# Optimization experiments

Measured on AMD Instinct MI355X. Metric: run time of the kernel, lower is better.

The kernel has to match this reference:

```python
import jax, jax.numpy as jnp
import numpy as np

B, T, D, H = 2, 2048, 1024, 16
HD = D // H  # 64


def setup_inputs() -> dict:
    key = jax.random.key(0)
    ks = jax.random.split(key, 9)
    w = lambda k, shp: (jax.random.normal(k, shp, jnp.float32) * 0.02)
    return {
        "x": jax.random.normal(ks[0], (B, T, D), jnp.float32),
        "Wq": w(ks[1], (D, D)), "bq": jnp.zeros((D,), jnp.float32),
        "Wk": w(ks[2], (D, D)), "bk": jnp.zeros((D,), jnp.float32),
        "Wv": w(ks[3], (D, D)), "bv": jnp.zeros((D,), jnp.float32),
        "Wo": w(ks[4], (D, D)), "bo": jnp.zeros((D,), jnp.float32),
        "Wqs": w(ks[5], (3, HD)), "bqs": jnp.zeros((3,), jnp.float32),
        "Wks": w(ks[6], (3, HD)), "bks": jnp.zeros((3,), jnp.float32),
        "Wvs": w(ks[7], (3, HD)), "bvs": jnp.zeros((3,), jnp.float32),
        "temp": jnp.float32(1.0),
    }


def reference(x, Wq, bq, Wk, bk, Wv, bv, Wo, bo, Wqs, bqs, Wks, bks, Wvs, bvs, temp):
    Bx, Tx, Dx = x.shape
    # project and split heads: [B,H,T,HD]
    split = lambda y: y.reshape(Bx, Tx, H, HD).transpose(0, 2, 1, 3)
    q = split(x @ Wq.T + bq)
    k = split(x @ Wk.T + bk)
    v = split(x @ Wv.T + bv)
    # STP projections to 3-d: [B,H,T,3]
    q_stp = q @ Wqs.T + bqs
    k3 = k @ Wks.T + bks
    v3 = v @ Wvs.T + bvs
    # cross-product term (note: original's layernormed k_sub/v_sub are dead code)
    cross_kv = jnp.cross(k3, v3, axis=-1)  # [B,H,T,3]
    scores = (jnp.einsum('bhqd,bhkd->bhqk', q, k)
              + jnp.einsum('bhqc,bhkc->bhqk', q_stp, cross_kv)) * temp
    attn = jax.nn.softmax(scores, axis=-1)
    out = jnp.einsum('bhqk,bhkd->bhqd', attn, v)  # [B,H,T,HD]
    out = out.transpose(0, 2, 1, 3).reshape(Bx, Tx, Dx)
    return out @ Wo.T + bo
```

## Files before the change

kernel.cpp:

```cpp
#include <hip/hip_runtime.h>
#include <stdint.h>

typedef unsigned short u16;
typedef unsigned int u32;
typedef __attribute__((ext_vector_type(8))) short bf16x8;
typedef __attribute__((ext_vector_type(4))) float f32x4;

__device__ __forceinline__ u16 f2b(float f) {
    union { float f; u32 u; } t; t.f = f;
    return (u16)((t.u + 0x7FFFu + ((t.u >> 16) & 1u)) >> 16);
}
__device__ __forceinline__ float b2f(u16 h) {
    union { u32 u; float f; } t; t.u = ((u32)h) << 16;
    return t.f;
}
__device__ __forceinline__ u32 pack2(float a, float b) {
    return (u32)f2b(a) | ((u32)f2b(b) << 16);
}

__device__ __forceinline__ void async_cp16(const u16* g, const u16* lds_base) {
    __builtin_amdgcn_global_load_lds(
        (const __attribute__((address_space(1))) void*)(uintptr_t)g,
        (__attribute__((address_space(3))) void*)(u32)(uintptr_t)lds_base,
        16, 0, 0);
}

__global__ void cast_all_kernel(const float* __restrict__ x,
                                const float* __restrict__ Wq, const float* __restrict__ Wk,
                                const float* __restrict__ Wv, const float* __restrict__ Wo,
                                u16* __restrict__ xb, u16* __restrict__ Wqb, u16* __restrict__ Wkb,
                                u16* __restrict__ Wvb, u16* __restrict__ Wob) {
    int i = blockIdx.x * blockDim.x + threadIdx.x;
    const float* s; u16* d; int off;
    if (i < 1048576) { s = x; d = xb; off = i; }
    else {
        int j = i - 1048576;
        int w = j >> 18; off = j & 262143;
        if (w == 0) { s = Wq; d = Wqb; }
        else if (w == 1) { s = Wk; d = Wkb; }
        else if (w == 2) { s = Wv; d = Wvb; }
        else { s = Wo; d = Wob; }
    }
    float4 f = ((const float4*)s)[off];
    ((uint2*)d)[off] = make_uint2(pack2(f.x, f.y), pack2(f.z, f.w));
}

#define GT 128
#define GK 32

template<int MODE>
__device__ __forceinline__ void gemm_core(
    const u16* __restrict__ A, const u16* __restrict__ W, const float* __restrict__ bias,
    u16* __restrict__ obf, u16* __restrict__ vtout, float* __restrict__ ofp)
{
    __shared__ __align__(16) u16 As[GT * GK];
    __shared__ __align__(16) u16 Bs[GT * GK];
    const int tid = threadIdx.x;
    const int lane = tid & 63, w = tid >> 6;
    const int wm = w >> 1, wn = w & 1;
    const int l15 = lane & 15, quad = lane >> 4;
    const int M0 = blockIdx.y * GT, N0 = blockIdx.x * GT;

    f32x4 acc[4][4];
#pragma unroll
    for (int i = 0; i < 4; i++)
#pragma unroll
        for (int j = 0; j < 4; j++) acc[i][j] = (f32x4){0.f, 0.f, 0.f, 0.f};

    int ua = w * 128 + lane;
    int r0 = ua >> 2, c0 = ((ua & 3) ^ (r0 & 3)) * 8;
    int ub = ua + 64;
    int r1 = ub >> 2, c1 = ((ub & 3) ^ (r1 & 3)) * 8;
    const u16* Ag0 = A + (size_t)(M0 + r0) * 1024 + c0;
    const u16* Ag1 = A + (size_t)(M0 + r1) * 1024 + c1;
    const u16* Wg0 = W + (size_t)(N0 + r0) * 1024 + c0;
    const u16* Wg1 = W + (size_t)(N0 + r1) * 1024 + c1;
    const u16* As0 = As + (w * 128) * 8;
    const u16* As1 = As + (w * 128 + 64) * 8;
    const u16* Bs0 = Bs + (w * 128) * 8;
    const u16* Bs1 = Bs + (w * 128 + 64) * 8;

    for (int k0 = 0; k0 < 1024; k0 += GK) {
        __syncthreads();
        async_cp16(Ag0 + k0, As0);
        async_cp16(Ag1 + k0, As1);
        async_cp16(Wg0 + k0, Bs0);
        async_cp16(Wg1 + k0, Bs1);
        __syncthreads();

        bf16x8 af[4], bf[4];
#pragma unroll
        for (int mi = 0; mi < 4; mi++)
            af[mi] = *(const bf16x8*)(As + (wm * 64 + mi * 16 + l15) * 32 + ((quad ^ (l15 & 3)) * 8));
#pragma unroll
        for (int ni = 0; ni < 4; ni++)
            bf[ni] = *(const bf16x8*)(Bs + (wn * 64 + ni * 16 + l15) * 32 + ((quad ^ (l15 & 3)) * 8));
#pragma unroll
        for (int mi = 0; mi < 4; mi++)
#pragma unroll
            for (int ni = 0; ni < 4; ni++)
                acc[mi][ni] = __builtin_amdgcn_mfma_f32_16x16x32_bf16(af[mi], bf[ni], acc[mi][ni], 0, 0, 0);
    }

#pragma unroll
    for (int mi = 0; mi < 4; mi++)
#pragma unroll
        for (int ni = 0; ni < 4; ni++) {
            int n = N0 + wn * 64 + ni * 16 + l15;
            float bias_n = bias[n];
            float vals[4];
#pragma unroll
            for (int r = 0; r < 4; r++)
                vals[r] = acc[mi][ni][r] + bias_n;
            int m0 = M0 + wm * 64 + mi * 16 + quad * 4;
            if (MODE == 0) {
                int b = m0 >> 11, t = m0 & 2047;
                int h = n >> 6, hd = n & 63;
#pragma unroll
                for (int r = 0; r < 4; r++)
                    obf[((size_t)((b * 16 + h) * 2048 + (t + r)) << 6) + hd] = f2b(vals[r]);
                if (vtout) {
                    *(uint2*)(vtout + ((size_t)((b * 16 + h) * 64 + hd)) * 2048 + t) =
                        make_uint2(pack2(vals[0], vals[1]), pack2(vals[2], vals[3]));
                }
            } else {
#pragma unroll
                for (int r = 0; r < 4; r++)
                    ofp[(size_t)(m0 + r) * 1024 + n] = vals[r];
            }
        }
}

__global__ __launch_bounds__(256) void gemm_qkv_kernel(
    const u16* __restrict__ xb,
    const u16* __restrict__ Wq, const u16* __restrict__ Wk, const u16* __restrict__ Wv,
    const float* __restrict__ bq, const float* __restrict__ bk, const float* __restrict__ bv,
    u16* __restrict__ q, u16* __restrict__ k, u16* __restrict__ v, u16* __restrict__ vT)
{
    const u16* W; const float* bias; u16* o; u16* vt = nullptr;
    if (blockIdx.z == 0)      { W = Wq; bias = bq; o = q; }
    else if (blockIdx.z == 1) { W = Wk; bias = bk; o = k; }
    else                      { W = Wv; bias = bv; o = v; vt = vT; }
    gemm_core<0>(xb, W, bias, o, vt, nullptr);
}

__global__ __launch_bounds__(256) void gemm_out_kernel(
    const u16* __restrict__ ao, const u16* __restrict__ Wo, const float* __restrict__ bo,
    float* __restrict__ out)
{
    gemm_core<1>(ao, Wo, bo, nullptr, nullptr, out);
}

__global__ void build_ext_kernel(
    const u16* __restrict__ q, const u16* __restrict__ k, const u16* __restrict__ v,
    const float* __restrict__ Wqs, const float* __restrict__ bqs,
    const float* __restrict__ Wks, const float* __restrict__ bks,
    const float* __restrict__ Wvs, const float* __restrict__ bvs,
    const float* __restrict__ temp_p,
    u16* __restrict__ qe, u16* __restrict__ ke)
{
    int row = blockIdx.x * blockDim.x + threadIdx.x;
    if (row >= 2 * 16 * 2048) return;
    const float temp = *temp_p * 1.44269504088896f;
    const u16* qr = q + (size_t)row * 64;
    const u16* kr = k + (size_t)row * 64;
    const u16* vr = v + (size_t)row * 64;

    float qs0 = bqs[0], qs1 = bqs[1], qs2 = bqs[2];
    float ks0 = bks[0], ks1 = bks[1], ks2 = bks[2];
    float vs0 = bvs[0], vs1 = bvs[1], vs2 = bvs[2];
#pragma unroll
    for (int j = 0; j < 64; j += 8) {
        bf16x8 qv = *(const bf16x8*)(qr + j);
        bf16x8 kv = *(const bf16x8*)(kr + j);
        bf16x8 vv = *(const bf16x8*)(vr + j);
#pragma unroll
        for (int i = 0; i < 8; i++) {
            float qf = b2f((u16)qv[i]);
            float kf = b2f((u16)kv[i]);
            float vf = b2f((u16)vv[i]);
            qs0 += qf * Wqs[j + i]; qs1 += qf * Wqs[64 + j + i]; qs2 += qf * Wqs[128 + j + i];
            ks0 += kf * Wks[j + i]; ks1 += kf * Wks[64 + j + i]; ks2 += kf * Wks[128 + j + i];
            vs0 += vf * Wvs[j + i]; vs1 += vf * Wvs[64 + j + i]; vs2 += vf * Wvs[128 + j + i];
        }
    }
    float c0 = ks1 * vs2 - ks2 * vs1;
    float c1 = ks2 * vs0 - ks0 * vs2;
    float c2 = ks0 * vs1 - ks1 * vs0;

    u16* qer = qe + (size_t)row * 96;
    u16* ker = ke + (size_t)row * 96;
#pragma unroll
    for (int j = 0; j < 64; j += 8) {
        bf16x8 qv = *(const bf16x8*)(qr + j);
        bf16x8 sq;
#pragma unroll
        for (int i = 0; i < 8; i++) sq[i] = (short)f2b(b2f((u16)qv[i]) * temp);
        *(bf16x8*)(qer + j) = sq;
        *(bf16x8*)(ker + j) = *(const bf16x8*)(kr + j);
    }
    *(uint2*)(qer + 64) = make_uint2(pack2(qs0 * temp, qs1 * temp), (u32)f2b(qs2 * temp));
    *(uint2*)(ker + 64) = make_uint2(pack2(c0, c1), (u32)f2b(c2));
    uint2 z = make_uint2(0u, 0u);
#pragma unroll
    for (int j = 68; j < 96; j += 4) {
        *(uint2*)(qer + j) = z;
        *(uint2*)(ker + j) = z;
    }
}

__global__ __launch_bounds__(256) void attn_kernel(
    const u16* __restrict__ qe, const u16* __restrict__ ke, const u16* __restrict__ vT,
    u16* __restrict__ out)
{
    __shared__ __align__(16) u16 Ks[64 * 128];
    __shared__ __align__(16) u16 Vt[64 * 64];
    __shared__ __align__(16) u16 Ps[128 * 64];

    const int tid = threadIdx.x;
    const int lane = tid & 63, w = tid >> 6;
    const int l15 = lane & 15, quad = lane >> 4;
    const int lsw = l15 & 7;
    const int bh = blockIdx.y;
    const int q0 = blockIdx.x * 128;

    const u16* qeb = qe + (size_t)bh * 2048 * 96;
    const u16* keb = ke + (size_t)bh * 2048 * 96;
    const u16* vTb = vT + (size_t)bh * 64 * 2048;

    bf16x8 bq[2][3];
#pragma unroll
    for (int s = 0; s < 2; s++) {
        const u16* qrow = qeb + (size_t)(q0 + w * 32 + s * 16 + l15) * 96;
#pragma unroll
        for (int ks = 0; ks < 3; ks++) bq[s][ks] = *(const bf16x8*)(qrow + ks * 32 + quad * 8);
    }

    f32x4 O[2][4];
    float l_part[2];
#pragma unroll
    for (int s = 0; s < 2; s++) {
        l_part[s] = 0.f;
#pragma unroll
        for (int dt = 0; dt < 4; dt++) O[s][dt] = (f32x4){0.f, 0.f, 0.f, 0.f};
    }

    const int srow = tid >> 2, spart = tid & 3;
    const int sh = srow & 7;
    u16* Pw[2];
#pragma unroll
    for (int s = 0; s < 2; s++) Pw[s] = Ps + (size_t)(w * 32 + s * 16 + l15) * 64;

    for (int kb = 0; kb < 2048; kb += 64) {
        const u16* kg = keb + (size_t)(kb + srow) * 96;
        uint4 kx0 = *(const uint4*)(kg + spart * 8);
        uint4 kx1 = *(const uint4*)(kg + (spart + 4) * 8);
        uint4 kx2 = *(const uint4*)(kg + (spart + 8) * 8);
        const u16* vg = vTb + (size_t)srow * 2048 + kb;
        uint4 vx0 = *(const uint4*)(vg + spart * 8);
        uint4 vx1 = *(const uint4*)(vg + (spart + 4) * 8);
        __syncthreads();
        *(uint4*)(Ks + srow * 128 + ((spart    ) ^ sh) * 8) = kx0;
        *(uint4*)(Ks + srow * 128 + ((spart + 4) ^ sh) * 8) = kx1;
        *(uint4*)(Ks + srow * 128 + ((spart + 8) ^ sh) * 8) = kx2;
        *(uint4*)(Vt + srow * 64 + ((spart    ) ^ sh) * 8) = vx0;
        *(uint4*)(Vt + srow * 64 + ((spart + 4) ^ sh) * 8) = vx1;
        __syncthreads();

        f32x4 S[2][4];
#pragma unroll
        for (int s = 0; s < 2; s++)
#pragma unroll
            for (int nt = 0; nt < 4; nt++) S[s][nt] = (f32x4){0.f, 0.f, 0.f, 0.f};
#pragma unroll
        for (int ks = 0; ks < 3; ks++) {
            bf16x8 ak[4];
#pragma unroll
            for (int nt = 0; nt < 4; nt++)
                ak[nt] = *(const bf16x8*)(Ks + (nt * 16 + l15) * 128 + (((ks * 4 + quad) ^ lsw) & 15) * 8);
#pragma unroll
            for (int s = 0; s < 2; s++)
#pragma unroll
                for (int nt = 0; nt < 4; nt++)
                    S[s][nt] = __builtin_amdgcn_mfma_f32_16x16x32_bf16(ak[nt], bq[s][ks], S[s][nt], 0, 0, 0);
        }

#pragma unroll
        for (int s = 0; s < 2; s++) {
            float sum = 0.f;
#pragma unroll
            for (int nt = 0; nt < 4; nt++)
#pragma unroll
                for (int r = 0; r < 4; r++) {
                    float p = __builtin_amdgcn_exp2f(S[s][nt][r]);
                    S[s][nt][r] = p;
                    sum += p;
                }
            l_part[s] += sum;
#pragma unroll
            for (int nt = 0; nt < 4; nt++) {
                int c = (nt * 2 + (quad >> 1)) ^ lsw;
                *(uint2*)(Pw[s] + c * 8 + (quad & 1) * 4) =
                    make_uint2(pack2(S[s][nt][0], S[s][nt][1]), pack2(S[s][nt][2], S[s][nt][3]));
            }
        }

#pragma unroll
        for (int kk = 0; kk < 2; kk++) {
            bf16x8 av[4];
#pragma unroll
            for (int dt = 0; dt < 4; dt++)
                av[dt] = *(const bf16x8*)(Vt + (dt * 16 + l15) * 64 + ((kk * 4 + quad) ^ lsw) * 8);
#pragma unroll
            for (int s = 0; s < 2; s++) {
                bf16x8 pb = *(const bf16x8*)(Pw[s] + ((kk * 4 + quad) ^ lsw) * 8);
#pragma unroll
                for (int dt = 0; dt < 4; dt++)
                    O[s][dt] = __builtin_amdgcn_mfma_f32_16x16x32_bf16(av[dt], pb, O[s][dt], 0, 0, 0);
            }
        }
    }

    const int b = bh >> 4, h = bh & 15;
#pragma unroll
    for (int s = 0; s < 2; s++) {
        float l = l_part[s];
        l += __shfl_xor(l, 16);
        l += __shfl_xor(l, 32);
        float linv = 1.0f / l;
        int tq = q0 + w * 32 + s * 16 + l15;
#pragma unroll
        for (int dt = 0; dt < 4; dt++) {
            int d = h * 64 + dt * 16 + quad * 4;
            *(uint2*)(out + (size_t)(b * 2048 + tq) * 1024 + d) =
                make_uint2(pack2(O[s][dt][0] * linv, O[s][dt][1] * linv),
                           pack2(O[s][dt][2] * linv, O[s][dt][3] * linv));
        }
    }
}

extern "C" void kernel_launch(void* const* d_in, const int* in_sizes, int n_in,
                              void* d_out, int out_size, void* d_ws, size_t ws_size,
                              hipStream_t stream)
{
    (void)in_sizes; (void)n_in; (void)out_size; (void)ws_size;
    const float* x   = (const float*)d_in[0];
    const float* Wq  = (const float*)d_in[1];
    const float* bq  = (const float*)d_in[2];
    const float* Wk  = (const float*)d_in[3];
    const float* bk  = (const float*)d_in[4];
    const float* Wv  = (const float*)d_in[5];
    const float* bv  = (const float*)d_in[6];
    const float* Wo  = (const float*)d_in[7];
    const float* bo  = (const float*)d_in[8];
    const float* Wqs = (const float*)d_in[9];
    const float* bqs = (const float*)d_in[10];
    const float* Wks = (const float*)d_in[11];
    const float* bks = (const float*)d_in[12];
    const float* Wvs = (const float*)d_in[13];
    const float* bvs = (const float*)d_in[14];
    const float* temp = (const float*)d_in[15];

    char* ws = (char*)d_ws;
    u16* xb  = (u16*)(ws);
    u16* Wqb = (u16*)(ws + 8388608);
    u16* Wkb = (u16*)(ws + 10485760);
    u16* Wvb = (u16*)(ws + 12582912);
    u16* Wob = (u16*)(ws + 14680064);
    u16* qb  = (u16*)(ws + 16777216);
    u16* kbq = (u16*)(ws + 25165824);
    u16* vbq = (u16*)(ws + 33554432);
    u16* qeb = (u16*)(ws + 41943040);
    u16* keb = (u16*)(ws + 54525952);
    u16* vTb = (u16*)(ws + 67108864);
    u16* aob = xb;

    cast_all_kernel<<<8192, 256, 0, stream>>>(x, Wq, Wk, Wv, Wo, xb, Wqb, Wkb, Wvb, Wob);
    gemm_qkv_kernel<<<dim3(8, 32, 3), 256, 0, stream>>>(xb, Wqb, Wkb, Wvb, bq, bk, bv, qb, kbq, vbq, vTb);
    build_ext_kernel<<<256, 256, 0, stream>>>(qb, kbq, vbq, Wqs, bqs, Wks, bks, Wvs, bvs, temp, qeb, keb);
    attn_kernel<<<dim3(16, 32), 256, 0, stream>>>(qeb, keb, vTb, aob);
    gemm_out_kernel<<<dim3(8, 32), 256, 0, stream>>>(aob, Wob, bo, (float*)d_out);
}
```

Baseline: 253.4 us.

## Fuse STP projections into QKV GEMM epilogue and shrink output GEMM tile

The QKV GEMM epilogue now computes the 3-d STP projections with a cross-lane shuffle reduction and writes the extended q/k rows and transposed V directly. This removes the separate q/k/v bf16 buffers and the build_ext pass that re-read them. A small finish kernel computes the k×v cross product from float4 side buffers. Separately, the output GEMM uses 64x128 tiles to launch twice as many blocks, trading less per-block reuse for better CU occupancy. The epilogue stores are scalar u16 writes with per-row zero padding, which may be less coalesced than before.

```diff
diff --git a/kernel.cpp b/kernel.cpp
--- a/kernel.cpp
+++ b/kernel.cpp
@@ -9,10 +9,6 @@
 __device__ __forceinline__ u16 f2b(float f) {
     union { float f; u32 u; } t; t.f = f;
     return (u16)((t.u + 0x7FFFu + ((t.u >> 16) & 1u)) >> 16);
-}
-__device__ __forceinline__ float b2f(u16 h) {
-    union { u32 u; float f; } t; t.u = ((u32)h) << 16;
-    return t.f;
 }
 __device__ __forceinline__ u32 pack2(float a, float b) {
     return (u32)f2b(a) | ((u32)f2b(b) << 16);
@@ -45,21 +41,30 @@
     ((uint2*)d)[off] = make_uint2(pack2(f.x, f.y), pack2(f.z, f.w));
 }
 
-#define GT 128
-#define GK 32
-
-template<int MODE>
-__device__ __forceinline__ void gemm_core(
-    const u16* __restrict__ A, const u16* __restrict__ W, const float* __restrict__ bias,
-    u16* __restrict__ obf, u16* __restrict__ vtout, float* __restrict__ ofp)
+__global__ __launch_bounds__(256) void gemm_qkv_kernel(
+    const u16* __restrict__ xb,
+    const u16* __restrict__ Wq, const u16* __restrict__ Wk, const u16* __restrict__ Wv,
+    const float* __restrict__ bq, const float* __restrict__ bk, const float* __restrict__ bv,
+    const float* __restrict__ Wqs, const float* __restrict__ bqs,
+    const float* __restrict__ Wks, const float* __restrict__ bks,
+    const float* __restrict__ Wvs, const float* __restrict__ bvs,
+    const float* __restrict__ temp_p,
+    u16* __restrict__ qe, u16* __restrict__ ke, u16* __restrict__ vT,
+    float4* __restrict__ k3b, float4* __restrict__ v3b)
 {
-    __shared__ __align__(16) u16 As[GT * GK];
-    __shared__ __align__(16) u16 Bs[GT * GK];
+    __shared__ __align__(16) u16 As[128 * 32];
+    __shared__ __align__(16) u16 Bs[128 * 32];
     const int tid = threadIdx.x;
     const int lane = tid & 63, w = tid >> 6;
     const int wm = w >> 1, wn = w & 1;
     const int l15 = lane & 15, quad = lane >> 4;
-    const int M0 = blockIdx.y * GT, N0 = blockIdx.x * GT;
+    const int M0 = blockIdx.y * 128, N0 = blockIdx.x * 128;
+    const int bz = blockIdx.z;
+
+    const u16* W = (bz == 0) ? Wq : (bz == 1) ? Wk : Wv;
+    const float* bias = (bz == 0) ? bq : (bz == 1) ? bk : bv;
+    const float* Wst = (bz == 0) ? Wqs : (bz == 1) ? Wks : Wvs;
+    const float* bst = (bz == 0) ? bqs : (bz == 1) ? bks : bvs;
 
     f32x4 acc[4][4];
 #pragma unroll
@@ -71,8 +76,8 @@
     int r0 = ua >> 2, c0 = ((ua & 3) ^ (r0 & 3)) * 8;
     int ub = ua + 64;
     int r1 = ub >> 2, c1 = ((ub & 3) ^ (r1 & 3)) * 8;
-    const u16* Ag0 = A + (size_t)(M0 + r0) * 1024 + c0;
-    const u16* Ag1 = A + (size_t)(M0 + r1) * 1024 + c1;
+    const u16* Ag0 = xb + (size_t)(M0 + r0) * 1024 + c0;
+    const u16* Ag1 = xb + (size_t)(M0 + r1) * 1024 + c1;
     const u16* Wg0 = W + (size_t)(N0 + r0) * 1024 + c0;
     const u16* Wg1 = W + (size_t)(N0 + r1) * 1024 + c1;
     const u16* As0 = As + (w * 128) * 8;
@@ -80,7 +85,7 @@
     const u16* Bs0 = Bs + (w * 128) * 8;
     const u16* Bs1 = Bs + (w * 128 + 64) * 8;
 
-    for (int k0 = 0; k0 < 1024; k0 += GK) {
+    for (int k0 = 0; k0 < 1024; k0 += 32) {
         __syncthreads();
         async_cp16(Ag0 + k0, As0);
         async_cp16(Ag1 + k0, As1);
@@ -102,111 +107,168 @@
                 acc[mi][ni] = __builtin_amdgcn_mfma_f32_16x16x32_bf16(af[mi], bf[ni], acc[mi][ni], 0, 0, 0);
     }
 
-#pragma unroll
-    for (int mi = 0; mi < 4; mi++)
-#pragma unroll
-        for (int ni = 0; ni < 4; ni++) {
-            int n = N0 + wn * 64 + ni * 16 + l15;
-            float bias_n = bias[n];
-            float vals[4];
-#pragma unroll
-            for (int r = 0; r < 4; r++)
-                vals[r] = acc[mi][ni][r] + bias_n;
-            int m0 = M0 + wm * 64 + mi * 16 + quad * 4;
-            if (MODE == 0) {
-                int b = m0 >> 11, t = m0 & 2047;
-                int h = n >> 6, hd = n & 63;
-#pragma unroll
-                for (int r = 0; r < 4; r++)
-                    obf[((size_t)((b * 16 + h) * 2048 + (t + r)) << 6) + hd] = f2b(vals[r]);
-                if (vtout) {
-                    *(uint2*)(vtout + ((size_t)((b * 16 + h) * 64 + hd)) * 2048 + t) =
-                        make_uint2(pack2(vals[0], vals[1]), pack2(vals[2], vals[3]));
+    const float tau = temp_p[0] * 1.44269504088896f;
+    const int nb = N0 + wn * 64;
+    const int h = nb >> 6;
+    float bias_v[4], wst_v[3][4];
+#pragma unroll
+    for (int ni = 0; ni < 4; ni++) {
+        bias_v[ni] = bias[nb + ni * 16 + l15];
+#pragma unroll
+        for (int c = 0; c < 3; c++) wst_v[c][ni] = Wst[c * 64 + ni * 16 + l15];
+    }
+    const float bst0 = bst[0], bst1 = bst[1], bst2 = bst[2];
+
+#pragma unroll
+    for (int mi = 0; mi < 4; mi++) {
+        int m0 = M0 + wm * 64 + mi * 16 + quad * 4;
+        int b = m0 >> 11, t0 = m0 & 2047;
+        float p0[4], p1[4], p2[4];
+#pragma unroll
+        for (int r = 0; r < 4; r++) {
+            float a0 = 0.f, a1 = 0.f, a2 = 0.f;
+#pragma unroll
+            for (int ni = 0; ni < 4; ni++) {
+                float v = acc[mi][ni][r] + bias_v[ni];
+                a0 += v * wst_v[0][ni];
+                a1 += v * wst_v[1][ni];
+                a2 += v * wst_v[2][ni];
+            }
+#pragma unroll
+            for (int off = 1; off < 16; off <<= 1) {
+                a0 += __shfl_xor(a0, off);
+                a1 += __shfl_xor(a1, off);
+                a2 += __shfl_xor(a2, off);
+            }
+            p0[r] = a0 + bst0; p1[r] = a1 + bst1; p2[r] = a2 + bst2;
+        }
+
+        if (bz == 0) {
+#pragma unroll
+            for (int r = 0; r < 4; r++) {
+                size_t row = (size_t)((b * 16 + h) * 2048 + (t0 + r));
+                u16* qer = qe + row * 96;
+#pragma unroll
+                for (int ni = 0; ni < 4; ni++)
+                    qer[ni * 16 + l15] = f2b((acc[mi][ni][r] + bias_v[ni]) * tau);
+                if (l15 == 0) {
+                    *(u32*)(qer + 64) = pack2(p0[r] * tau, p1[r] * tau);
+                    *(u32*)(qer + 66) = (u32)f2b(p2[r] * tau);
+                    uint2 z = make_uint2(0u, 0u);
+#pragma unroll
+                    for (int j = 68; j < 96; j += 4) *(uint2*)(qer + j) = z;
                 }
-            } else {
-#pragma unroll
-                for (int r = 0; r < 4; r++)
-                    ofp[(size_t)(m0 + r) * 1024 + n] = vals[r];
-            }
-        }
-}
-
-__global__ __launch_bounds__(256) void gemm_qkv_kernel(
-    const u16* __restrict__ xb,
-    const u16* __restrict__ Wq, const u16* __restrict__ Wk, const u16* __restrict__ Wv,
-    const float* __restrict__ bq, const float* __restrict__ bk, const float* __restrict__ bv,
-    u16* __restrict__ q, u16* __restrict__ k, u16* __restrict__ v, u16* __restrict__ vT)
+            }
+        } else if (bz == 1) {
+#pragma unroll
+            for (int r = 0; r < 4; r++) {
+                size_t row = (size_t)((b * 16 + h) * 2048 + (t0 + r));
+                u16* ker = ke + row * 96;
+#pragma unroll
+                for (int ni = 0; ni < 4; ni++)
+                    ker[ni * 16 + l15] = f2b(acc[mi][ni][r] + bias_v[ni]);
+                if (l15 == 0)
+                    k3b[row] = make_float4(p0[r], p1[r], p2[r], 0.f);
+            }
+        } else {
+#pragma unroll
+            for (int ni = 0; ni < 4; ni++) {
+                int hd = ni * 16 + l15;
+                float v0 = acc[mi][ni][0] + bias_v[ni];
+                float v1 = acc[mi][ni][1] + bias_v[ni];
+                float v2 = acc[mi][ni][2] + bias_v[ni];
+                float v3 = acc[mi][ni][3] + bias_v[ni];
+                *(uint2*)(vT + ((size_t)((b * 16 + h) * 64 + hd)) * 2048 + t0) =
+                    make_uint2(pack2(v0, v1), pack2(v2, v3));
+            }
+            if (l15 == 0) {
+#pragma unroll
+                for (int r = 0; r < 4; r++) {
+                    size_t row = (size_t)((b * 16 + h) * 2048 + (t0 + r));
+                    v3b[row] = make_float4(p0[r], p1[r], p2[r], 0.f);
+                }
+            }
+        }
+    }
+}
+
+__global__ void finish_ext_kernel(const float4* __restrict__ k3b, const float4* __restrict__ v3b,
+                                  u16* __restrict__ ke)
 {
-    const u16* W; const float* bias; u16* o; u16* vt = nullptr;
-    if (blockIdx.z == 0)      { W = Wq; bias = bq; o = q; }
-    else if (blockIdx.z == 1) { W = Wk; bias = bk; o = k; }
-    else                      { W = Wv; bias = bv; o = v; vt = vT; }
-    gemm_core<0>(xb, W, bias, o, vt, nullptr);
+    int row = blockIdx.x * blockDim.x + threadIdx.x;
+    if (row >= 2 * 16 * 2048) return;
+    float4 k3 = k3b[row];
+    float4 v3 = v3b[row];
+    float c0 = k3.y * v3.z - k3.z * v3.y;
+    float c1 = k3.z * v3.x - k3.x * v3.z;
+    float c2 = k3.x * v3.y - k3.y * v3.x;
+    u16* ker = ke + (size_t)row * 96;
+    *(u32*)(ker + 64) = pack2(c0, c1);
+    *(u32*)(ker + 66) = (u32)f2b(c2);
+    uint2 z = make_uint2(0u, 0u);
+#pragma unroll
+    for (int j = 68; j < 96; j += 4) *(uint2*)(ker + j) = z;
 }
 
 __global__ __launch_bounds__(256) void gemm_out_kernel(
     const u16* __restrict__ ao, const u16* __restrict__ Wo, const float* __restrict__ bo,
     float* __restrict__ out)
 {
-    gemm_core<1>(ao, Wo, bo, nullptr, nullptr, out);
-}
-
-__global__ void build_ext_kernel(
-    const u16* __restrict__ q, const u16* __restrict__ k, const u16* __restrict__ v,
-    const float* __restrict__ Wqs, const float* __restrict__ bqs,
-    const float* __restrict__ Wks, const float* __restrict__ bks,
-    const float* __restrict__ Wvs, const float* __restrict__ bvs,
-    const float* __restrict__ temp_p,
-    u16* __restrict__ qe, u16* __restrict__ ke)
-{
-    int row = blockIdx.x * blockDim.x + threadIdx.x;
-    if (row >= 2 * 16 * 2048) return;
-    const float temp = *temp_p * 1.44269504088896f;
-    const u16* qr = q + (size_t)row * 64;
-    const u16* kr = k + (size_t)row * 64;
-    const u16* vr = v + (size_t)row * 64;
-
-    float qs0 = bqs[0], qs1 = bqs[1], qs2 = bqs[2];
-    float ks0 = bks[0], ks1 = bks[1], ks2 = bks[2];
-    float vs0 = bvs[0], vs1 = bvs[1], vs2 = bvs[2];
-#pragma unroll
-    for (int j = 0; j < 64; j += 8) {
-        bf16x8 qv = *(const bf16x8*)(qr + j);
-        bf16x8 kv = *(const bf16x8*)(kr + j);
-        bf16x8 vv = *(const bf16x8*)(vr + j);
-#pragma unroll
-        for (int i = 0; i < 8; i++) {
-            float qf = b2f((u16)qv[i]);
-            float kf = b2f((u16)kv[i]);
-            float vf = b2f((u16)vv[i]);
-            qs0 += qf * Wqs[j + i]; qs1 += qf * Wqs[64 + j + i]; qs2 += qf * Wqs[128 + j + i];
-            ks0 += kf * Wks[j + i]; ks1 += kf * Wks[64 + j + i]; ks2 += kf * Wks[128 + j + i];
-            vs0 += vf * Wvs[j + i]; vs1 += vf * Wvs[64 + j + i]; vs2 += vf * Wvs[128 + j + i];
-        }
-    }
-    float c0 = ks1 * vs2 - ks2 * vs1;
-    float c1 = ks2 * vs0 - ks0 * vs2;
-    float c2 = ks0 * vs1 - ks1 * vs0;
-
-    u16* qer = qe + (size_t)row * 96;
-    u16* ker = ke + (size_t)row * 96;
-#pragma unroll
-    for (int j = 0; j < 64; j += 8) {
-        bf16x8 qv = *(const bf16x8*)(qr + j);
-        bf16x8 sq;
-#pragma unroll
-        for (int i = 0; i < 8; i++) sq[i] = (short)f2b(b2f((u16)qv[i]) * temp);
-        *(bf16x8*)(qer + j) = sq;
-        *(bf16x8*)(ker + j) = *(const bf16x8*)(kr + j);
-    }
-    *(uint2*)(qer + 64) = make_uint2(pack2(qs0 * temp, qs1 * temp), (u32)f2b(qs2 * temp));
-    *(uint2*)(ker + 64) = make_uint2(pack2(c0, c1), (u32)f2b(c2));
-    uint2 z = make_uint2(0u, 0u);
-#pragma unroll
-    for (int j = 68; j < 96; j += 4) {
-        *(uint2*)(qer + j) = z;
-        *(uint2*)(ker + j) = z;
-    }
+    __shared__ __align__(16) u16 As[64 * 32];
+    __shared__ __align__(16) u16 Bs[128 * 32];
+    const int tid = threadIdx.x;
+    const int lane = tid & 63, w = tid >> 6;
+    const int wm = w >> 1, wn = w & 1;
+    const int l15 = lane & 15, quad = lane >> 4;
+    const int M0 = blockIdx.y * 64, N0 = blockIdx.x * 128;
+
+    f32x4 acc[2][4];
+#pragma unroll
+    for (int i = 0; i < 2; i++)
+#pragma unroll
+        for (int j = 0; j < 4; j++) acc[i][j] = (f32x4){0.f, 0.f, 0.f, 0.f};
+
+    int ra = tid >> 2, ca = ((tid & 3) ^ (ra & 3)) * 8;
+    int rb1 = ra + 64;
+    const u16* Aga = ao + (size_t)(M0 + ra) * 1024 + ca;
+    const u16* Bg0 = Wo + (size_t)(N0 + ra) * 1024 + ca;
+    const u16* Bg1 = Wo + (size_t)(N0 + rb1) * 1024 + ca;
+    const u16* Asb = As + (w * 64) * 8;
+    const u16* Bs0 = Bs + (w * 64) * 8;
+    const u16* Bs1 = Bs + (256 + w * 64) * 8;
+
+    for (int k0 = 0; k0 < 1024; k0 += 32) {
+        __syncthreads();
+        async_cp16(Aga + k0, Asb);
+        async_cp16(Bg0 + k0, Bs0);
+        async_cp16(Bg1 + k0, Bs1);
+        __syncthreads();
+
+        bf16x8 af[2], bf[4];
+#pragma unroll
+        for (int mi = 0; mi < 2; mi++)
+            af[mi] = *(const bf16x8*)(As + (wm * 32 + mi * 16 + l15) * 32 + ((quad ^ (l15 & 3)) * 8));
+#pragma unroll
+        for (int ni = 0; ni < 4; ni++)
+            bf[ni] = *(const bf16x8*)(Bs + (wn * 64 + ni * 16 + l15) * 32 + ((quad ^ (l15 & 3)) * 8));
+#pragma unroll
+        for (int mi = 0; mi < 2; mi++)
+#pragma unroll
+            for (int ni = 0; ni < 4; ni++)
+                acc[mi][ni] = __builtin_amdgcn_mfma_f32_16x16x32_bf16(af[mi], bf[ni], acc[mi][ni], 0, 0, 0);
+    }
+
+#pragma unroll
+    for (int mi = 0; mi < 2; mi++)
+#pragma unroll
+        for (int ni = 0; ni < 4; ni++) {
+            int n = N0 + wn * 64 + ni * 16 + l15;
+            float bias_n = bo[n];
+            int m0 = M0 + wm * 32 + mi * 16 + quad * 4;
+#pragma unroll
+            for (int r = 0; r < 4; r++)
+                out[(size_t)(m0 + r) * 1024 + n] = acc[mi][ni][r] + bias_n;
+        }
 }
 
 __global__ __launch_bounds__(256) void attn_kernel(
@@ -367,17 +429,18 @@
     u16* Wkb = (u16*)(ws + 10485760);
     u16* Wvb = (u16*)(ws + 12582912);
     u16* Wob = (u16*)(ws + 14680064);
-    u16* qb  = (u16*)(ws + 16777216);
-    u16* kbq = (u16*)(ws + 25165824);
-    u16* vbq = (u16*)(ws + 33554432);
-    u16* qeb = (u16*)(ws + 41943040);
-    u16* keb = (u16*)(ws + 54525952);
-    u16* vTb = (u16*)(ws + 67108864);
-    u16* aob = xb;
+    u16* qeb = (u16*)(ws + 16777216);
+    u16* keb = (u16*)(ws + 29360128);
+    u16* vTb = (u16*)(ws + 41943040);
+    float4* k3b = (float4*)(ws + 50331648);
+    float4* v3b = (float4*)(ws + 51380224);
+    u16* aob = (u16*)(ws + 52428800);
 
     cast_all_kernel<<<8192, 256, 0, stream>>>(x, Wq, Wk, Wv, Wo, xb, Wqb, Wkb, Wvb, Wob);
-    gemm_qkv_kernel<<<dim3(8, 32, 3), 256, 0, stream>>>(xb, Wqb, Wkb, Wvb, bq, bk, bv, qb, kbq, vbq, vTb);
-    build_ext_kernel<<<256, 256, 0, stream>>>(qb, kbq, vbq, Wqs, bqs, Wks, bks, Wvs, bvs, temp, qeb, keb);
+    gemm_qkv_kernel<<<dim3(8, 32, 3), 256, 0, stream>>>(
+        xb, Wqb, Wkb, Wvb, bq, bk, bv, Wqs, bqs, Wks, bks, Wvs, bvs, temp,
+        qeb, keb, vTb, k3b, v3b);
+    finish_ext_kernel<<<256, 256, 0, stream>>>(k3b, v3b, keb);
     attn_kernel<<<dim3(16, 32), 256, 0, stream>>>(qeb, keb, vTb, aob);
-    gemm_out_kernel<<<dim3(8, 32), 256, 0, stream>>>(aob, Wob, bo, (float*)d_out);
-}
+    gemm_out_kernel<<<dim3(8, 64), 256, 0, stream>>>(aob, Wob, bo, (float*)d_out);
+}
```

Result: no change. 249.0 us (-1.7%).
